# Kernel tuning notes

Measured on AMD Instinct MI355X. Metric: run time of the kernel, lower is better.

The kernel has to match this reference:

```python
import jax, jax.numpy as jnp
import numpy as np

N = 8192        # nodes
E = 49152       # edges (~avg degree 6, triangular mesh)
H = 6           # GATv2 heads
C = 512         # hidden_size (per-head out channels)
F_IN = 2 + C    # GATv2 in_channels = coord(2) + hidden(512)
ALL_FEAT = 37   # deform_in_c-2 + 16 + 16
NUM_LOOP = 3
LRELU_SLOPE = 0.2


def setup_inputs() -> dict:
    key = jax.random.key(0)
    ks = jax.random.split(key, 10)
    x = jax.random.uniform(ks[0], (N, 7), dtype=jnp.float32)
    local_feat = jax.random.normal(ks[1], (N, 16), dtype=jnp.float32)
    conv_feat = jax.random.normal(ks[2], (N, 16), dtype=jnp.float32)
    edge_index = jax.random.randint(ks[3], (2, E), 0, N, dtype=jnp.int64)
    bd_mask = jnp.zeros((N,), jnp.int32)  # poly_mesh=False path
    W_lin = jax.random.normal(ks[4], (ALL_FEAT, C), dtype=jnp.float32) / np.float32(np.sqrt(ALL_FEAT))
    b_lin = jnp.zeros((C,), jnp.float32)
    Wl = jax.random.normal(ks[5], (F_IN, H * C), dtype=jnp.float32) / np.float32(np.sqrt(F_IN))
    Wr = jax.random.normal(ks[6], (F_IN, H * C), dtype=jnp.float32) / np.float32(np.sqrt(F_IN))
    att = jax.random.normal(ks[7], (H, C), dtype=jnp.float32) / np.float32(np.sqrt(C))
    gat_bias = jnp.zeros((C,), jnp.float32)
    W_coord = jax.random.normal(ks[8], (C, 2), dtype=jnp.float32) / np.float32(np.sqrt(C))
    b_coord = jnp.zeros((2,), jnp.float32)
    return dict(x=x, local_feat=local_feat, conv_feat=conv_feat,
                W_lin=W_lin, b_lin=b_lin, Wl=Wl, Wr=Wr, att=att,
                gat_bias=gat_bias, W_coord=W_coord, b_coord=b_coord,
                edge_index=edge_index, bd_mask=bd_mask)


def _gatv2(feat, src, dst, Wl, Wr, att, bias):
    # PyG GATv2Conv: lin_l on source, lin_r on target, additive attention
    n = feat.shape[0]
    xl = (feat @ Wl).reshape(n, H, C)            # source-side transform
    xr = (feat @ Wr).reshape(n, H, C)            # target-side transform
    e = xl[src] + xr[dst]                        # [E', H, C]
    e = jax.nn.leaky_relu(e, LRELU_SLOPE)
    logits = jnp.einsum('ehc,hc->eh', e, att)    # [E', H]
    m = jax.ops.segment_max(logits, dst, num_segments=n)
    m = jnp.where(jnp.isfinite(m), m, 0.0)
    a = jnp.exp(logits - m[dst])
    denom = jax.ops.segment_sum(a, dst, num_segments=n) + 1e-16
    alpha = a / denom[dst]                       # segment softmax over incoming edges
    msg = xl[src] * alpha[:, :, None]            # [E', H, C]
    out = jax.ops.segment_sum(msg, dst, num_segments=n)  # [N, H, C]
    return out.mean(axis=1) + bias               # concat=False -> mean over heads


def reference(x, local_feat, conv_feat, W_lin, b_lin, Wl, Wr, att, gat_bias,
              W_coord, b_coord, edge_index, bd_mask):
    coord = x[:, :2]
    hidden_in = jnp.concatenate([x[:, 2:], local_feat, conv_feat], axis=1)
    hidden = jax.nn.selu(hidden_in @ W_lin + b_lin)
    # GATv2Conv adds self-loops by default
    loops = jnp.arange(N, dtype=edge_index.dtype)
    src = jnp.concatenate([edge_index[0], loops])
    dst = jnp.concatenate([edge_index[1], loops])
    for _ in range(NUM_LOOP):
        up = coord[:, 0] == 1.0
        down = coord[:, 0] == 0.0
        left = coord[:, 1] == 0.0
        right = coord[:, 1] == 1.0
        feat = jnp.concatenate([coord, hidden], axis=1)   # [N, 514]
        hidden = jax.nn.selu(_gatv2(feat, src, dst, Wl, Wr, att, gat_bias))
        out = hidden @ W_coord + b_coord                  # [N, 2]
        ox = jnp.where(down, 0.0, jnp.where(up, 1.0, out[:, 0]))
        oy = jnp.where(right, 1.0, jnp.where(left, 0.0, out[:, 1]))
        coord = jnp.stack([ox, oy], axis=1)
    return coord
```

## Files before the change

### kernel.cpp

```cpp
#include <hip/hip_runtime.h>
#include <hip/hip_bf16.h>
#include <math.h>

#define N_NODES   8192
#define NUM_E     49152
#define NUM_EDGES (NUM_E + N_NODES)
#define H_HEADS   6
#define C_DIM     512
#define HC        (H_HEADS * C_DIM)
#define XLR       (2 * HC)
#define N_FEAT    37
#define LRELU_SLOPE 0.2f
#define SELU_LAMBDA 1.0507009873554805f
#define SELU_ALPHA  1.6732632423543772f

typedef __bf16 bf16_t;
typedef bf16_t bf16x8 __attribute__((ext_vector_type(8)));
typedef float  f32x4  __attribute__((ext_vector_type(4)));
typedef float  f32x2  __attribute__((ext_vector_type(2)));

__device__ __forceinline__ int edge_src(const int* ei, int e) {
    return e < NUM_E ? ei[e] : (e - NUM_E);
}
__device__ __forceinline__ int edge_dst(const int* ei, int e) {
    return e < NUM_E ? ei[NUM_E + e] : (e - NUM_E);
}
__device__ __forceinline__ float selu_f(float v) {
    return v > 0.f ? SELU_LAMBDA * v : SELU_LAMBDA * SELU_ALPHA * (__expf(v) - 1.f);
}
__device__ __forceinline__ void gload_lds16(const void* g, void* l) {
    __builtin_amdgcn_global_load_lds((const __attribute__((address_space(1))) void*)g,
                                     (__attribute__((address_space(3))) void*)l, 16, 0, 0);
}

__global__ __launch_bounds__(512) void k_hidden0(
    const float* __restrict__ x, const float* __restrict__ lf,
    const float* __restrict__ cf, const float* __restrict__ W,
    const float* __restrict__ b, bf16_t* __restrict__ hidden,
    float* __restrict__ coord)
{
    int n = blockIdx.x;
    int c = threadIdx.x;
    __shared__ float f[N_FEAT];
    if (c < 5)            f[c] = x[n*7 + 2 + c];
    else if (c < 21)      f[c] = lf[n*16 + (c-5)];
    else if (c < N_FEAT)  f[c] = cf[n*16 + (c-21)];
    if (c < 2) coord[n*2 + c] = x[n*7 + c];
    __syncthreads();
    float acc = b[c];
    #pragma unroll
    for (int k = 0; k < N_FEAT; ++k) acc = fmaf(f[k], W[k*C_DIM + c], acc);
    hidden[n*C_DIM + c] = (bf16_t)selu_f(acc);
}

__global__ __launch_bounds__(256) void k_wt_transpose(const float* __restrict__ W,
                                                      bf16_t* __restrict__ WT)
{
    __shared__ float tile[32][33];
    int k0 = blockIdx.y * 32;
    int n0 = blockIdx.x * 32;
    int tx = threadIdx.x & 31, ty = threadIdx.x >> 5;
    #pragma unroll
    for (int i = 0; i < 4; ++i)
        tile[ty + i*8][tx] = W[(size_t)(k0 + 2 + ty + i*8) * HC + n0 + tx];
    __syncthreads();
    #pragma unroll
    for (int i = 0; i < 4; ++i)
        WT[(size_t)(n0 + ty + i*8) * C_DIM + k0 + tx] = (bf16_t)tile[tx][ty + i*8];
}

__global__ void k_hist(const int* __restrict__ ei, int* __restrict__ counts) {
    int e = blockIdx.x * blockDim.x + threadIdx.x;
    if (e >= NUM_EDGES) return;
    atomicAdd(&counts[edge_dst(ei, e)], 1);
}

__global__ __launch_bounds__(256) void k_scan(const int* __restrict__ counts,
                                              int* __restrict__ row_ptr,
                                              int* __restrict__ cursor) {
    __shared__ int part[256];
    __shared__ int off[257];
    int t = threadIdx.x;
    int base = t * 32;
    int local[32];
    int s = 0;
    #pragma unroll
    for (int i = 0; i < 32; ++i) { local[i] = s; s += counts[base + i]; }
    part[t] = s;
    __syncthreads();
    if (t == 0) {
        off[0] = 0;
        for (int i = 0; i < 256; ++i) off[i+1] = off[i] + part[i];
    }
    __syncthreads();
    int o = off[t];
    #pragma unroll
    for (int i = 0; i < 32; ++i) {
        int v = o + local[i];
        row_ptr[base + i] = v;
        cursor[base + i]  = v;
    }
    if (t == 255) row_ptr[N_NODES] = off[256];
}

__global__ void k_scatter(const int* __restrict__ ei, int* __restrict__ cursor,
                          int* __restrict__ csr_eid) {
    int e = blockIdx.x * blockDim.x + threadIdx.x;
    if (e >= NUM_EDGES) return;
    int pos = atomicAdd(&cursor[edge_dst(ei, e)], 1);
    csr_eid[pos] = e;
}

#define GM 128
#define GN 128
#define GK 32
__global__ __launch_bounds__(256) void k_gemm_bf16(
    const bf16_t* __restrict__ A,
    const bf16_t* __restrict__ BT,
    const float*  __restrict__ Wl,
    const float*  __restrict__ Wr,
    const float*  __restrict__ coord,
    bf16_t* __restrict__ out)
{
    __shared__ bf16_t As[2][GM][GK];
    __shared__ bf16_t Bs[2][GM][GK];
    int tid  = threadIdx.x;
    int wave = tid >> 6;
    int lane = tid & 63;
    int rowBase = blockIdx.y * GM;
    int colBase = blockIdx.x * GN;
    int wr = (wave >> 1) * 64;
    int wc = (wave & 1) * 64;

    f32x4 acc[4][4] = {};

    int gsw = (((lane & 3) ^ ((lane >> 3) & 3))) * 8;
    const bf16_t* Ag = A  + (size_t)(rowBase + wave*32 + (lane >> 2)) * C_DIM + gsw;
    const bf16_t* Bg = BT + (size_t)(colBase + wave*32 + (lane >> 2)) * C_DIM + gsw;
    int m16 = lane & 15;
    int q8s = (((lane >> 4) ^ ((lane >> 1) & 3))) * 8;

    gload_lds16(Ag,            &As[0][wave*32     ][0]);
    gload_lds16(Ag + 16*C_DIM, &As[0][wave*32 + 16][0]);
    gload_lds16(Bg,            &Bs[0][wave*32     ][0]);
    gload_lds16(Bg + 16*C_DIM, &Bs[0][wave*32 + 16][0]);

    int p = 0;
    for (int k0 = 0; k0 < C_DIM; k0 += GK) {
        __syncthreads();
        if (k0 + GK < C_DIM) {
            gload_lds16(Ag + k0 + GK,            &As[p^1][wave*32     ][0]);
            gload_lds16(Ag + k0 + GK + 16*C_DIM, &As[p^1][wave*32 + 16][0]);
            gload_lds16(Bg + k0 + GK,            &Bs[p^1][wave*32     ][0]);
            gload_lds16(Bg + k0 + GK + 16*C_DIM, &Bs[p^1][wave*32 + 16][0]);
        }
        bf16x8 af[4], bfr[4];
        #pragma unroll
        for (int i = 0; i < 4; ++i) af[i]  = *(const bf16x8*)&As[p][wr + i*16 + m16][q8s];
        #pragma unroll
        for (int j = 0; j < 4; ++j) bfr[j] = *(const bf16x8*)&Bs[p][wc + j*16 + m16][q8s];
        #pragma unroll
        for (int i = 0; i < 4; ++i)
            #pragma unroll
            for (int j = 0; j < 4; ++j)
                acc[i][j] = __builtin_amdgcn_mfma_f32_16x16x32_bf16(af[i], bfr[j], acc[i][j], 0, 0, 0);
        p ^= 1;
    }

    const float* Wtop = (colBase < HC) ? Wl : Wr;
    int coff = (colBase < HC) ? 0 : HC;

    int ccol  = lane & 15;
    int crow4 = (lane >> 4) * 4;
    #pragma unroll
    for (int i = 0; i < 4; ++i) {
        #pragma unroll
        for (int r = 0; r < 4; ++r) {
            int row = rowBase + wr + i*16 + crow4 + r;
            float c0 = coord[row*2 + 0], c1 = coord[row*2 + 1];
            size_t rb = (size_t)row * XLR;
            #pragma unroll
            for (int j = 0; j < 4; ++j) {
                int col = colBase + wc + j*16 + ccol;
                int wcol = col - coff;
                out[rb + col] = (bf16_t)(acc[i][j][r] + c0 * Wtop[wcol] + c1 * Wtop[HC + wcol]);
            }
        }
    }
}

#define MAX_DEG 128
__global__ __launch_bounds__(384) void k_attn_agg(
    const bf16_t* __restrict__ xlr,
    const int* __restrict__ row_ptr, const int* __restrict__ csr_eid,
    const int* __restrict__ ei, const float* __restrict__ att,
    const float* __restrict__ gat_bias, const float* __restrict__ W_coord,
    const float* __restrict__ b_coord, const float* __restrict__ coord_in,
    bf16_t* __restrict__ hidden, float* __restrict__ coord_out)
{
    int n = blockIdx.x;
    int tid = threadIdx.x;
    int h = tid >> 6, lane = tid & 63;
    __shared__ int   s_src[MAX_DEG];
    __shared__ float s_acc[HC];
    __shared__ float s_red[12];

    int beg = row_ptr[n];
    int deg = min(row_ptr[n + 1] - beg, MAX_DEG);
    for (int j = tid; j < deg; j += 384) s_src[j] = edge_src(ei, csr_eid[beg + j]);
    __syncthreads();

    size_t off = (size_t)h * C_DIM + lane * 8;
    bf16x8 xrv = *(const bf16x8*)(xlr + (size_t)n * XLR + HC + off);
    f32x2 xr2[4], at2[4], ac2[4] = {};
    #pragma unroll
    for (int i = 0; i < 4; ++i) {
        xr2[i] = f32x2{(float)xrv[2*i], (float)xrv[2*i+1]};
        at2[i] = f32x2{att[off + 2*i], att[off + 2*i + 1]};
    }

    float l = 0.f;
    int j = 0;
    for (; j + 2 <= deg; j += 2) {
        bf16x8 xa = *(const bf16x8*)(xlr + (size_t)s_src[j]     * XLR + off);
        bf16x8 xb = *(const bf16x8*)(xlr + (size_t)s_src[j + 1] * XLR + off);
        f32x2 xla[4], xlb[4];
        #pragma unroll
        for (int i = 0; i < 4; ++i) {
            xla[i] = f32x2{(float)xa[2*i], (float)xa[2*i+1]};
            xlb[i] = f32x2{(float)xb[2*i], (float)xb[2*i+1]};
        }
        f32x2 sa = {0.f, 0.f}, sb = {0.f, 0.f};
        #pragma unroll
        for (int i = 0; i < 4; ++i) {
            f32x2 va = xla[i] + xr2[i];
            f32x2 vb = xlb[i] + xr2[i];
            sa += __builtin_elementwise_max(va, va * LRELU_SLOPE) * at2[i];
            sb += __builtin_elementwise_max(vb, vb * LRELU_SLOPE) * at2[i];
        }
        float suma = sa.x + sa.y, sumb = sb.x + sb.y;
        #pragma unroll
        for (int o = 1; o < 64; o <<= 1) {
            suma += __shfl_xor(suma, o);
            sumb += __shfl_xor(sumb, o);
        }
        float aa = __expf(suma), ab = __expf(sumb);
        l += aa + ab;
        #pragma unroll
        for (int i = 0; i < 4; ++i) ac2[i] += aa * xla[i] + ab * xlb[i];
    }
    if (j < deg) {
        bf16x8 xa = *(const bf16x8*)(xlr + (size_t)s_src[j] * XLR + off);
        f32x2 xla[4];
        #pragma unroll
        for (int i = 0; i < 4; ++i) xla[i] = f32x2{(float)xa[2*i], (float)xa[2*i+1]};
        f32x2 sa = {0.f, 0.f};
        #pragma unroll
        for (int i = 0; i < 4; ++i) {
            f32x2 va = xla[i] + xr2[i];
            sa += __builtin_elementwise_max(va, va * LRELU_SLOPE) * at2[i];
        }
        float suma = sa.x + sa.y;
        #pragma unroll
        for (int o = 1; o < 64; o <<= 1) suma += __shfl_xor(suma, o);
        float aa = __expf(suma);
        l += aa;
        #pragma unroll
        for (int i = 0; i < 4; ++i) ac2[i] += aa * xla[i];
    }

    float invl = 1.f / (l + 1e-16f) * (1.f / 6.f);
    #pragma unroll
    for (int i = 0; i < 4; ++i) {
        s_acc[off + 2*i]     = ac2[i].x * invl;
        s_acc[off + 2*i + 1] = ac2[i].y * invl;
    }
    __syncthreads();

    float p0 = 0.f, p1 = 0.f;
    for (int c = tid; c < C_DIM; c += 384) {
        float s = 0.f;
        #pragma unroll
        for (int hh = 0; hh < H_HEADS; ++hh) s += s_acc[hh * C_DIM + c];
        float hv = selu_f(s + gat_bias[c]);
        hidden[n * C_DIM + c] = (bf16_t)hv;
        p0 = fmaf(hv, W_coord[c * 2 + 0], p0);
        p1 = fmaf(hv, W_coord[c * 2 + 1], p1);
    }
    #pragma unroll
    for (int o = 32; o > 0; o >>= 1) { p0 += __shfl_down(p0, o); p1 += __shfl_down(p1, o); }
    if (lane == 0) { s_red[h * 2] = p0; s_red[h * 2 + 1] = p1; }
    __syncthreads();
    if (tid == 0) {
        float o0 = b_coord[0], o1 = b_coord[1];
        #pragma unroll
        for (int w = 0; w < H_HEADS; ++w) { o0 += s_red[w * 2]; o1 += s_red[w * 2 + 1]; }
        float cx = coord_in[n * 2 + 0], cy = coord_in[n * 2 + 1];
        float ox = (cx == 0.0f) ? 0.f : ((cx == 1.0f) ? 1.f : o0);
        float oy = (cy == 1.0f) ? 1.f : ((cy == 0.0f) ? 0.f : o1);
        coord_out[n * 2 + 0] = ox;
        coord_out[n * 2 + 1] = oy;
    }
}

extern "C" void kernel_launch(void* const* d_in, const int* in_sizes, int n_in,
                              void* d_out, int out_size, void* d_ws, size_t ws_size,
                              hipStream_t stream)
{
    const float* x       = (const float*)d_in[0];
    const float* lf      = (const float*)d_in[1];
    const float* cf      = (const float*)d_in[2];
    const float* W_lin   = (const float*)d_in[3];
    const float* b_lin   = (const float*)d_in[4];
    const float* Wl      = (const float*)d_in[5];
    const float* Wr      = (const float*)d_in[6];
    const float* att     = (const float*)d_in[7];
    const float* gbias   = (const float*)d_in[8];
    const float* W_coord = (const float*)d_in[9];
    const float* b_coord = (const float*)d_in[10];
    const int*   ei      = (const int*)d_in[11];

    char* w = (char*)d_ws;
    auto alloc = [&](size_t bytes) { char* p = w; w += (bytes + 255) & ~255ull; return p; };
    bf16_t*   hidden  = (bf16_t*)alloc((size_t)N_NODES * C_DIM * 2);
    bf16_t*   WT      = (bf16_t*)alloc((size_t)XLR * C_DIM * 2);
    bf16_t*   xlr     = (bf16_t*)alloc((size_t)N_NODES * XLR * 2);
    int*      counts  = (int*)alloc((size_t)N_NODES * 4);
    int*      row_ptr = (int*)alloc((size_t)(N_NODES + 1) * 4);
    int*      cursor  = (int*)alloc((size_t)N_NODES * 4);
    int*      csr_eid = (int*)alloc((size_t)NUM_EDGES * 4);
    float*    cA      = (float*)alloc((size_t)N_NODES * 2 * 4);
    float*    cB      = (float*)alloc((size_t)N_NODES * 2 * 4);

    hipMemsetAsync(counts, 0, (size_t)N_NODES * 4, stream);
    k_hidden0<<<N_NODES, 512, 0, stream>>>(x, lf, cf, W_lin, b_lin, hidden, cA);
    {
        dim3 tg(HC / 32, C_DIM / 32);
        k_wt_transpose<<<tg, 256, 0, stream>>>(Wl, WT);
        k_wt_transpose<<<tg, 256, 0, stream>>>(Wr, WT + (size_t)HC * C_DIM);
    }
    k_hist<<<(NUM_EDGES + 255) / 256, 256, 0, stream>>>(ei, counts);
    k_scan<<<1, 256, 0, stream>>>(counts, row_ptr, cursor);
    k_scatter<<<(NUM_EDGES + 255) / 256, 256, 0, stream>>>(ei, cursor, csr_eid);

    float* cin = cA;
    for (int it = 0; it < 3; ++it) {
        float* cout = (it == 2) ? (float*)d_out : ((it == 0) ? cB : cA);
        dim3 g(XLR / GN, N_NODES / GM);
        k_gemm_bf16<<<g, 256, 0, stream>>>(hidden, WT, Wl, Wr, cin, xlr);
        k_attn_agg<<<N_NODES, 384, 0, stream>>>(xlr, row_ptr, csr_eid, ei, att,
                                                gbias, W_coord, b_coord, cin, hidden, cout);
        cin = cout;
    }
}
```

Measured before the change: 586.3 us.

## Retile bf16 GEMM to 256x256x64 with deeper prefetch pipeline and swizzled LDS

Replaces the 128x128x32, 4-wave GEMM with a 256x256x64, 8-wave kernel that uses 128KB of XOR-swizzled LDS. A phased software pipeline prefetches A one K-tile ahead and B two K-tiles ahead, with explicit vmcnt/lgkmcnt waits, barriers and setprio around the MFMA bursts. It also remaps block IDs to group tiles for L2 locality and hoists the Wl/Wr coordinate-term loads out of the epilogue loop. The aim is higher MFMA utilisation and less global and LDS traffic per FLOP. The cost is that only one workgroup fits per CU and the hand-placed waits and barriers are fragile.

```diff
diff --git a/kernel.cpp b/kernel.cpp
--- a/kernel.cpp
+++ b/kernel.cpp
@@ -111,10 +111,14 @@
     csr_eid[pos] = e;
 }
 
-#define GM 128
-#define GN 128
-#define GK 32
-__global__ __launch_bounds__(256) void k_gemm_bf16(
+#define BM 256
+#define BN 256
+#define BK 64
+#define NT (C_DIM / BK)
+#define NBX (XLR / BN)
+#define NWG ((N_NODES / BM) * NBX)
+
+__global__ __launch_bounds__(512, 2) void k_gemm_bf16(
     const bf16_t* __restrict__ A,
     const bf16_t* __restrict__ BT,
     const float*  __restrict__ Wl,
@@ -122,68 +126,129 @@
     const float*  __restrict__ coord,
     bf16_t* __restrict__ out)
 {
-    __shared__ bf16_t As[2][GM][GK];
-    __shared__ bf16_t Bs[2][GM][GK];
-    int tid  = threadIdx.x;
-    int wave = tid >> 6;
-    int lane = tid & 63;
-    int rowBase = blockIdx.y * GM;
-    int colBase = blockIdx.x * GN;
-    int wr = (wave >> 1) * 64;
-    int wc = (wave & 1) * 64;
-
-    f32x4 acc[4][4] = {};
-
-    int gsw = (((lane & 3) ^ ((lane >> 3) & 3))) * 8;
-    const bf16_t* Ag = A  + (size_t)(rowBase + wave*32 + (lane >> 2)) * C_DIM + gsw;
-    const bf16_t* Bg = BT + (size_t)(colBase + wave*32 + (lane >> 2)) * C_DIM + gsw;
-    int m16 = lane & 15;
-    int q8s = (((lane >> 4) ^ ((lane >> 1) & 3))) * 8;
-
-    gload_lds16(Ag,            &As[0][wave*32     ][0]);
-    gload_lds16(Ag + 16*C_DIM, &As[0][wave*32 + 16][0]);
-    gload_lds16(Bg,            &Bs[0][wave*32     ][0]);
-    gload_lds16(Bg + 16*C_DIM, &Bs[0][wave*32 + 16][0]);
-
-    int p = 0;
-    for (int k0 = 0; k0 < C_DIM; k0 += GK) {
-        __syncthreads();
-        if (k0 + GK < C_DIM) {
-            gload_lds16(Ag + k0 + GK,            &As[p^1][wave*32     ][0]);
-            gload_lds16(Ag + k0 + GK + 16*C_DIM, &As[p^1][wave*32 + 16][0]);
-            gload_lds16(Bg + k0 + GK,            &Bs[p^1][wave*32     ][0]);
-            gload_lds16(Bg + k0 + GK + 16*C_DIM, &Bs[p^1][wave*32 + 16][0]);
-        }
-        bf16x8 af[4], bfr[4];
-        #pragma unroll
-        for (int i = 0; i < 4; ++i) af[i]  = *(const bf16x8*)&As[p][wr + i*16 + m16][q8s];
-        #pragma unroll
-        for (int j = 0; j < 4; ++j) bfr[j] = *(const bf16x8*)&Bs[p][wc + j*16 + m16][q8s];
-        #pragma unroll
-        for (int i = 0; i < 4; ++i)
+    __shared__ __align__(1024) char smem[131072];
+    char* sA = smem;
+    char* sB = smem + 65536;
+
+    const int tid  = threadIdx.x;
+    const int wave = tid >> 6;
+    const int lane = tid & 63;
+    const int wm   = wave >> 2;
+    const int wn   = wave & 3;
+
+    int bid = blockIdx.y * gridDim.x + blockIdx.x;
+    bid = (bid & 7) * (NWG / 8) + (bid >> 3);
+    const int rowBase = (bid / NBX) * BM;
+    const int colBase = (bid % NBX) * BN;
+
+    const int rtid = tid >> 3;
+    const int csw  = ((tid & 7) * 8) ^ (((tid >> 3) & 7) << 3);
+    const bf16_t* pA = A  + (size_t)(rowBase + rtid) * C_DIM + csw;
+    const bf16_t* pB = BT + (size_t)(colBase + rtid) * C_DIM + csw;
+
+    auto stageA = [&](int t, int h) {
+        char* l = sA + ((t & 1) << 15) + (h << 14) + (wave << 10);
+        const bf16_t* g = pA + (size_t)(h * 128) * C_DIM + t * BK;
+        gload_lds16(g,              l);
+        gload_lds16(g + 64 * C_DIM, l + 8192);
+    };
+    auto stageB = [&](int t, int h) {
+        char* l = sB + ((t & 1) << 15) + (h << 14) + (wave << 10);
+        const bf16_t* g = pB + (size_t)(h * 128) * C_DIM + t * BK;
+        gload_lds16(g,              l);
+        gload_lds16(g + 64 * C_DIM, l + 8192);
+    };
+
+    stageB(0, 0); stageB(0, 1); stageA(0, 0); stageA(0, 1);
+    stageB(1, 0); stageB(1, 1);
+    __builtin_amdgcn_sched_barrier(0);
+    asm volatile("s_waitcnt vmcnt(4)" ::: "memory");
+    __builtin_amdgcn_sched_barrier(0);
+    __builtin_amdgcn_s_barrier();
+    __builtin_amdgcn_sched_barrier(0);
+
+    const int kb  = (lane >> 4) << 4;
+    const int sw  = (lane & 7) << 4;
+    const int xt0 = kb ^ sw;
+    const int xt1 = (64 | kb) ^ sw;
+    const int aRowOff = (wm * 128 + (lane & 15)) * 128;
+    const int bRowOff = (wn * 64  + (lane & 15)) * 128;
+
+    f32x4 acc[8][4] = {};
+
+    #pragma unroll 2
+    for (int t = 0; t < NT; ++t) {
+        const char* aP = sA + ((t & 1) << 15) + aRowOff;
+        const char* bP = sB + ((t & 1) << 15) + bRowOff;
+        bf16x8 bfv[4][2];
+
+        #pragma unroll
+        for (int ph = 0; ph < 4; ++ph) {
+            if (ph == 0)      { if (t + 1 < NT) stageA(t + 1, 0); }
+            else if (ph == 1) { if (t + 1 < NT) stageA(t + 1, 1); }
+            else if (ph == 2) { if (t + 2 < NT) stageB(t + 2, 0); }
+            else              { if (t + 2 < NT) stageB(t + 2, 1); }
+
+            if (ph == 0) {
+                #pragma unroll
+                for (int nf = 0; nf < 4; ++nf) {
+                    bfv[nf][0] = *(const bf16x8*)(bP + nf * 2048 + xt0);
+                    bfv[nf][1] = *(const bf16x8*)(bP + nf * 2048 + xt1);
+                }
+            }
+            bf16x8 af0k0 = *(const bf16x8*)(aP + (2*ph)     * 2048 + xt0);
+            bf16x8 af0k1 = *(const bf16x8*)(aP + (2*ph)     * 2048 + xt1);
+            bf16x8 af1k0 = *(const bf16x8*)(aP + (2*ph + 1) * 2048 + xt0);
+            bf16x8 af1k1 = *(const bf16x8*)(aP + (2*ph + 1) * 2048 + xt1);
+
+            __builtin_amdgcn_s_setprio(1);
             #pragma unroll
-            for (int j = 0; j < 4; ++j)
-                acc[i][j] = __builtin_amdgcn_mfma_f32_16x16x32_bf16(af[i], bfr[j], acc[i][j], 0, 0, 0);
-        p ^= 1;
+            for (int nf = 0; nf < 4; ++nf) {
+                acc[2*ph  ][nf] = __builtin_amdgcn_mfma_f32_16x16x32_bf16(af0k0, bfv[nf][0], acc[2*ph  ][nf], 0, 0, 0);
+                acc[2*ph+1][nf] = __builtin_amdgcn_mfma_f32_16x16x32_bf16(af1k0, bfv[nf][0], acc[2*ph+1][nf], 0, 0, 0);
+            }
+            #pragma unroll
+            for (int nf = 0; nf < 4; ++nf) {
+                acc[2*ph  ][nf] = __builtin_amdgcn_mfma_f32_16x16x32_bf16(af0k1, bfv[nf][1], acc[2*ph  ][nf], 0, 0, 0);
+                acc[2*ph+1][nf] = __builtin_amdgcn_mfma_f32_16x16x32_bf16(af1k1, bfv[nf][1], acc[2*ph+1][nf], 0, 0, 0);
+            }
+            __builtin_amdgcn_s_setprio(0);
+
+            if (ph == 3) {
+                __builtin_amdgcn_sched_barrier(0);
+                if (t < NT - 2)       asm volatile("s_waitcnt vmcnt(4)" ::: "memory");
+                else if (t == NT - 2) asm volatile("s_waitcnt vmcnt(0)" ::: "memory");
+            }
+            __builtin_amdgcn_sched_barrier(0);
+            asm volatile("s_waitcnt lgkmcnt(0)" ::: "memory");
+            __builtin_amdgcn_s_barrier();
+            __builtin_amdgcn_sched_barrier(0);
+        }
     }
 
     const float* Wtop = (colBase < HC) ? Wl : Wr;
-    int coff = (colBase < HC) ? 0 : HC;
-
-    int ccol  = lane & 15;
-    int crow4 = (lane >> 4) * 4;
-    #pragma unroll
-    for (int i = 0; i < 4; ++i) {
+    const int coff = (colBase < HC) ? 0 : HC;
+    const int ccol  = lane & 15;
+    const int crow4 = (lane >> 4) * 4;
+
+    float wv0[4], wv1[4];
+    #pragma unroll
+    for (int nf = 0; nf < 4; ++nf) {
+        int wcol = colBase + wn*64 + nf*16 + ccol - coff;
+        wv0[nf] = Wtop[wcol];
+        wv1[nf] = Wtop[HC + wcol];
+    }
+    #pragma unroll
+    for (int mf = 0; mf < 8; ++mf) {
         #pragma unroll
         for (int r = 0; r < 4; ++r) {
-            int row = rowBase + wr + i*16 + crow4 + r;
+            int row = rowBase + wm*128 + mf*16 + crow4 + r;
             float c0 = coord[row*2 + 0], c1 = coord[row*2 + 1];
             size_t rb = (size_t)row * XLR;
             #pragma unroll
-            for (int j = 0; j < 4; ++j) {
-                int col = colBase + wc + j*16 + ccol;
-                int wcol = col - coff;
-                out[rb + col] = (bf16_t)(acc[i][j][r] + c0 * Wtop[wcol] + c1 * Wtop[HC + wcol]);
+            for (int nf = 0; nf < 4; ++nf) {
+                int col = colBase + wn*64 + nf*16 + ccol;
+                out[rb + col] = (bf16_t)(acc[mf][nf][r] + c0 * wv0[nf] + c1 * wv1[nf]);
             }
         }
     }
@@ -346,8 +411,8 @@
     float* cin = cA;
     for (int it = 0; it < 3; ++it) {
         float* cout = (it == 2) ? (float*)d_out : ((it == 0) ? cB : cA);
-        dim3 g(XLR / GN, N_NODES / GM);
-        k_gemm_bf16<<<g, 256, 0, stream>>>(hidden, WT, Wl, Wr, cin, xlr);
+        dim3 g(NBX, N_NODES / BM);
+        k_gemm_bf16<<<g, 512, 0, stream>>>(hidden, WT, Wl, Wr, cin, xlr);
         k_attn_agg<<<N_NODES, 384, 0, stream>>>(xlr, row_ptr, csr_eid, ei, att,
                                                 gbias, W_coord, b_coord, cin, hidden, cout);
         cin = cout;
```

Result: faster. 554.4 us (-5.4%).
